# Kernel optimization log

Measured on AMD Instinct MI355X. Metric: run time of the kernel, lower is better.

The kernel has to match this reference:

```python
import jax, jax.numpy as jnp
import numpy as np


def _dwconv3(x, w, b):
    # Depthwise conv1d, kernel=3, 'same' padding, channels_first.
    # x: [B, Cs, L], w: [3, Cs], b: [Cs]
    xp = jnp.pad(x, ((0, 0), (0, 0), (1, 1)))
    return (w[0][:, None] * xp[:, :, :-2]
            + w[1][:, None] * xp[:, :, 1:-1]
            + w[2][:, None] * xp[:, :, 2:]
            + b[:, None])


def setup_inputs() -> dict:
    key = jax.random.key(0)
    ks = jax.random.split(key, 3)
    B, C, L, S = 32, 256, 4096, 8
    return {
        "inputs": jax.random.normal(ks[0], (B, C, L), jnp.float32),
        "conv_w": jax.random.normal(ks[1], (S, 3, C // S), jnp.float32) * 0.3,
        "conv_b": jnp.zeros((S, C // S), jnp.float32),
        "ln_gamma": jnp.ones((L,), jnp.float32),
        "ln_beta": jnp.zeros((L,), jnp.float32),
        "pw_w": jax.random.normal(ks[2], (C,), jnp.float32) * 0.3,
        "pw_b": jnp.zeros((C,), jnp.float32),
    }


def reference(inputs, conv_w, conv_b, ln_gamma, ln_beta, pw_w, pw_b):
    S = conv_w.shape[0]
    xs = jnp.split(inputs, S, axis=1)  # each [B, C/S, L]
    # sequential recurrence: y_i = dwconv_i(x_i + y_{i-1})
    y = _dwconv3(xs[0], conv_w[0], conv_b[0])
    ys = [y]
    for i in range(1, S):
        y = _dwconv3(xs[i] + y, conv_w[i], conv_b[i])
        ys.append(y)
    y = jnp.concatenate(ys, axis=1)  # [B, C, L]
    # keras LayerNormalization(axis=-1): normalize over time axis L
    mean = jnp.mean(y, axis=-1, keepdims=True)
    var = jnp.var(y, axis=-1, keepdims=True)
    y = (y - mean) * jax.lax.rsqrt(var + 1e-6) * ln_gamma + ln_beta
    # depthwise k=1 conv (per-channel scale + bias) then exact gelu
    y = jax.nn.gelu(y * pw_w[None, :, None] + pw_b[None, :, None], approximate=False)
    return inputs + y
```

## Files before the change

### kernel.cpp

```cpp
#include <hip/hip_runtime.h>
#include <math.h>

#define BB   32
#define CC   256
#define LL   4096
#define SS   8
#define CS   32
#define NT   512
#define NW   (NT / 64)
#define F4_ROW (LL / 4)
#define F4_THR (F4_ROW / NT)

__device__ __forceinline__ float gelu_exact(float x) {
    return 0.5f * x * (1.0f + erff(x * 0.70710678118654752440f));
}

__global__ __launch_bounds__(NT, 8)
void hdconv_encoder_kernel(const float* __restrict__ inp,
                           const float* __restrict__ conv_w,
                           const float* __restrict__ conv_b,
                           const float* __restrict__ ln_g,
                           const float* __restrict__ ln_b,
                           const float* __restrict__ pw_w,
                           const float* __restrict__ pw_b,
                           float* __restrict__ out) {
    __shared__ float4 S4[F4_ROW];
    __shared__ float  red[2 * NW];

    const int t    = threadIdx.x;
    const int blk  = blockIdx.x;
    const int b    = blk >> 5;
    const int c    = blk & 31;
    const int lane = t & 63;
    const int wave = t >> 6;

    float y[4 * F4_THR];
#pragma unroll
    for (int j = 0; j < 4 * F4_THR; ++j) y[j] = 0.0f;

    const float4* gp = (const float4*)ln_g;
    const float4* ep = (const float4*)ln_b;

    for (int i = 0; i < SS; ++i) {
        const int ch = i * CS + c;
        const float4* xrow = (const float4*)(inp + ((size_t)(b * CC + ch)) * LL);
        float4*       orow = (float4*)(out + ((size_t)(b * CC + ch)) * LL);

        float4 x4[F4_THR];
#pragma unroll
        for (int k = 0; k < F4_THR; ++k) x4[k] = xrow[t + NT * k];
        float4 g4[F4_THR], e4[F4_THR];
#pragma unroll
        for (int k = 0; k < F4_THR; ++k) {
            g4[k] = gp[t + NT * k];
            e4[k] = ep[t + NT * k];
        }
#pragma unroll
        for (int k = 0; k < F4_THR; ++k) {
            float4 s;
            s.x = x4[k].x + y[4 * k + 0];
            s.y = x4[k].y + y[4 * k + 1];
            s.z = x4[k].z + y[4 * k + 2];
            s.w = x4[k].w + y[4 * k + 3];
            S4[t + NT * k] = s;
        }
        __syncthreads();

        const float w0 = conv_w[i * 96 + 0 * CS + c];
        const float w1 = conv_w[i * 96 + 1 * CS + c];
        const float w2 = conv_w[i * 96 + 2 * CS + c];
        const float bb = conv_b[i * CS + c];

        float lsum = 0.0f, lsq = 0.0f;
#pragma unroll
        for (int k = 0; k < F4_THR; ++k) {
            const int f = t + NT * k;
            const float4 cc = S4[f];
            const float4 fm = S4[(f > 0) ? (f - 1) : 0];
            const float4 fp = S4[(f < F4_ROW - 1) ? (f + 1) : (F4_ROW - 1)];
            const float sm1 = (f > 0)          ? fm.w : 0.0f;
            const float sp4 = (f < F4_ROW - 1) ? fp.x : 0.0f;
            float y0 = fmaf(w0, sm1,  fmaf(w1, cc.x, fmaf(w2, cc.y, bb)));
            float y1 = fmaf(w0, cc.x, fmaf(w1, cc.y, fmaf(w2, cc.z, bb)));
            float y2 = fmaf(w0, cc.y, fmaf(w1, cc.z, fmaf(w2, cc.w, bb)));
            float y3 = fmaf(w0, cc.z, fmaf(w1, cc.w, fmaf(w2, sp4, bb)));
            y[4 * k + 0] = y0; y[4 * k + 1] = y1;
            y[4 * k + 2] = y2; y[4 * k + 3] = y3;
            lsum += (y0 + y1) + (y2 + y3);
            lsq  += fmaf(y0, y0, fmaf(y1, y1, fmaf(y2, y2, y3 * y3)));
        }

#pragma unroll
        for (int off = 32; off > 0; off >>= 1) {
            lsum += __shfl_down(lsum, off, 64);
            lsq  += __shfl_down(lsq,  off, 64);
        }
        if (lane == 0) { red[wave * 2] = lsum; red[wave * 2 + 1] = lsq; }
        __syncthreads();

        float sum = 0.0f, sq = 0.0f;
#pragma unroll
        for (int w = 0; w < NW; ++w) {
            sum += red[2 * w];
            sq  += red[2 * w + 1];
        }
        const float mean = sum * (1.0f / LL);
        const float var  = sq * (1.0f / LL) - mean * mean;
        const float inv  = rsqrtf(var + 1e-6f);

        const float pw = pw_w[ch];
        const float pb = pw_b[ch];
#pragma unroll
        for (int k = 0; k < F4_THR; ++k) {
            float4 o;
            float n;
            n   = fmaf((y[4 * k + 0] - mean) * inv, g4[k].x, e4[k].x);
            o.x = x4[k].x + gelu_exact(fmaf(n, pw, pb));
            n   = fmaf((y[4 * k + 1] - mean) * inv, g4[k].y, e4[k].y);
            o.y = x4[k].y + gelu_exact(fmaf(n, pw, pb));
            n   = fmaf((y[4 * k + 2] - mean) * inv, g4[k].z, e4[k].z);
            o.z = x4[k].z + gelu_exact(fmaf(n, pw, pb));
            n   = fmaf((y[4 * k + 3] - mean) * inv, g4[k].w, e4[k].w);
            o.w = x4[k].w + gelu_exact(fmaf(n, pw, pb));
            orow[t + NT * k] = o;
        }
    }
}

extern "C" void kernel_launch(void* const* d_in, const int* in_sizes, int n_in,
                              void* d_out, int out_size, void* d_ws, size_t ws_size,
                              hipStream_t stream) {
    const float* inp    = (const float*)d_in[0];
    const float* conv_w = (const float*)d_in[1];
    const float* conv_b = (const float*)d_in[2];
    const float* ln_g   = (const float*)d_in[3];
    const float* ln_b   = (const float*)d_in[4];
    const float* pw_w   = (const float*)d_in[5];
    const float* pw_b   = (const float*)d_in[6];
    float* out = (float*)d_out;

    dim3 grid(BB * CS);
    dim3 block(NT);
    hdconv_encoder_kernel<<<grid, block, 0, stream>>>(
        inp, conv_w, conv_b, ln_g, ln_b, pw_w, pw_b, out);
}
```

Before: 257.8 us.

## Halve block size, prefetch next split's input, use shuffles for conv halos

Halves the block to 256 threads so each thread holds 16 elements. The input row for the next split is prefetched into registers while the current split is processed, so the load overlaps the stencil, LayerNorm and GELU work. The full-row LDS staging of the convolution input is dropped: neighbor values now come from wave shuffles, with a small LDS seam array for wave boundaries, and barriers are replaced by a custom waitcnt-plus-barrier. The cost is higher register pressure, which may lower occupancy, and fewer threads per block.

```diff
diff --git a/kernel.cpp b/kernel.cpp
--- a/kernel.cpp
+++ b/kernel.cpp
@@ -6,16 +6,21 @@
 #define LL   4096
 #define SS   8
 #define CS   32
-#define NT   512
+#define NT   256
 #define NW   (NT / 64)
 #define F4_ROW (LL / 4)
 #define F4_THR (F4_ROW / NT)
+#define NSEG  (NW * F4_THR)
 
 __device__ __forceinline__ float gelu_exact(float x) {
     return 0.5f * x * (1.0f + erff(x * 0.70710678118654752440f));
 }
 
-__global__ __launch_bounds__(NT, 8)
+__device__ __forceinline__ void bar_lds() {
+    asm volatile("s_waitcnt lgkmcnt(0)\n\ts_barrier" ::: "memory");
+}
+
+__global__ __launch_bounds__(NT, 4)
 void hdconv_encoder_kernel(const float* __restrict__ inp,
                            const float* __restrict__ conv_w,
                            const float* __restrict__ conv_b,
@@ -24,8 +29,9 @@
                            const float* __restrict__ pw_w,
                            const float* __restrict__ pw_b,
                            float* __restrict__ out) {
-    __shared__ float4 S4[F4_ROW];
-    __shared__ float  red[2 * NW];
+    __shared__ float seamW[NSEG + 1];
+    __shared__ float seamX[NSEG + 1];
+    __shared__ float red[2 * NW];
 
     const int t    = threadIdx.x;
     const int blk  = blockIdx.x;
@@ -34,37 +40,57 @@
     const int lane = t & 63;
     const int wave = t >> 6;
 
-    float y[4 * F4_THR];
+    if (t == 0) { seamW[0] = 0.0f; seamX[NSEG] = 0.0f; }
+
+    float y[16];
 #pragma unroll
-    for (int j = 0; j < 4 * F4_THR; ++j) y[j] = 0.0f;
+    for (int j = 0; j < 16; ++j) y[j] = 0.0f;
 
-    const float4* gp = (const float4*)ln_g;
-    const float4* ep = (const float4*)ln_b;
-
-    for (int i = 0; i < SS; ++i) {
-        const int ch = i * CS + c;
-        const float4* xrow = (const float4*)(inp + ((size_t)(b * CC + ch)) * LL);
-        float4*       orow = (float4*)(out + ((size_t)(b * CC + ch)) * LL);
-
-        float4 x4[F4_THR];
-#pragma unroll
-        for (int k = 0; k < F4_THR; ++k) x4[k] = xrow[t + NT * k];
-        float4 g4[F4_THR], e4[F4_THR];
+    float4 g4[F4_THR], e4[F4_THR];
+    {
+        const float4* gp = (const float4*)ln_g;
+        const float4* ep = (const float4*)ln_b;
 #pragma unroll
         for (int k = 0; k < F4_THR; ++k) {
             g4[k] = gp[t + NT * k];
             e4[k] = ep[t + NT * k];
         }
+    }
+
+    float4 xc[F4_THR];
+    {
+        const float4* xrow = (const float4*)(inp + ((size_t)(b * CC + c)) * LL);
+#pragma unroll
+        for (int k = 0; k < F4_THR; ++k) xc[k] = xrow[t + NT * k];
+    }
+
+    for (int i = 0; i < SS; ++i) {
+        const int ch = i * CS + c;
+        float4* orow = (float4*)(out + ((size_t)(b * CC + ch)) * LL);
+
+        const int inext = (i < SS - 1) ? (i + 1) : i;
+        const float4* xnrow = (const float4*)(inp + ((size_t)(b * CC + inext * CS + c)) * LL);
+        float4 xn[F4_THR];
+#pragma unroll
+        for (int k = 0; k < F4_THR; ++k) xn[k] = xnrow[t + NT * k];
+
+        float4 s4[F4_THR];
 #pragma unroll
         for (int k = 0; k < F4_THR; ++k) {
-            float4 s;
-            s.x = x4[k].x + y[4 * k + 0];
-            s.y = x4[k].y + y[4 * k + 1];
-            s.z = x4[k].z + y[4 * k + 2];
-            s.w = x4[k].w + y[4 * k + 3];
-            S4[t + NT * k] = s;
+            s4[k].x = xc[k].x + y[4 * k + 0];
+            s4[k].y = xc[k].y + y[4 * k + 1];
+            s4[k].z = xc[k].z + y[4 * k + 2];
+            s4[k].w = xc[k].w + y[4 * k + 3];
         }
-        __syncthreads();
+        if (lane == 63) {
+#pragma unroll
+            for (int k = 0; k < F4_THR; ++k) seamW[1 + (k * NW + wave)] = s4[k].w;
+        }
+        if (lane == 0) {
+#pragma unroll
+            for (int k = 0; k < F4_THR; ++k) seamX[k * NW + wave] = s4[k].x;
+        }
+        bar_lds();
 
         const float w0 = conv_w[i * 96 + 0 * CS + c];
         const float w1 = conv_w[i * 96 + 1 * CS + c];
@@ -74,12 +100,12 @@
         float lsum = 0.0f, lsq = 0.0f;
 #pragma unroll
         for (int k = 0; k < F4_THR; ++k) {
-            const int f = t + NT * k;
-            const float4 cc = S4[f];
-            const float4 fm = S4[(f > 0) ? (f - 1) : 0];
-            const float4 fp = S4[(f < F4_ROW - 1) ? (f + 1) : (F4_ROW - 1)];
-            const float sm1 = (f > 0)          ? fm.w : 0.0f;
-            const float sp4 = (f < F4_ROW - 1) ? fp.x : 0.0f;
+            const int j = k * NW + wave;
+            float sm1 = __shfl_up(s4[k].w, 1);
+            float sp4 = __shfl_down(s4[k].x, 1);
+            if (lane == 0)  sm1 = seamW[j];
+            if (lane == 63) sp4 = seamX[j + 1];
+            const float4 cc = s4[k];
             float y0 = fmaf(w0, sm1,  fmaf(w1, cc.x, fmaf(w2, cc.y, bb)));
             float y1 = fmaf(w0, cc.x, fmaf(w1, cc.y, fmaf(w2, cc.z, bb)));
             float y2 = fmaf(w0, cc.y, fmaf(w1, cc.z, fmaf(w2, cc.w, bb)));
@@ -96,7 +122,7 @@
             lsq  += __shfl_down(lsq,  off, 64);
         }
         if (lane == 0) { red[wave * 2] = lsum; red[wave * 2 + 1] = lsq; }
-        __syncthreads();
+        bar_lds();
 
         float sum = 0.0f, sq = 0.0f;
 #pragma unroll
@@ -115,15 +141,18 @@
             float4 o;
             float n;
             n   = fmaf((y[4 * k + 0] - mean) * inv, g4[k].x, e4[k].x);
-            o.x = x4[k].x + gelu_exact(fmaf(n, pw, pb));
+            o.x = xc[k].x + gelu_exact(fmaf(n, pw, pb));
             n   = fmaf((y[4 * k + 1] - mean) * inv, g4[k].y, e4[k].y);
-            o.y = x4[k].y + gelu_exact(fmaf(n, pw, pb));
+            o.y = xc[k].y + gelu_exact(fmaf(n, pw, pb));
             n   = fmaf((y[4 * k + 2] - mean) * inv, g4[k].z, e4[k].z);
-            o.z = x4[k].z + gelu_exact(fmaf(n, pw, pb));
+            o.z = xc[k].z + gelu_exact(fmaf(n, pw, pb));
             n   = fmaf((y[4 * k + 3] - mean) * inv, g4[k].w, e4[k].w);
-            o.w = x4[k].w + gelu_exact(fmaf(n, pw, pb));
+            o.w = xc[k].w + gelu_exact(fmaf(n, pw, pb));
             orow[t + NT * k] = o;
         }
+
+#pragma unroll
+        for (int k = 0; k < F4_THR; ++k) xc[k] = xn[k];
     }
 }
 
```

Result: slower. 284.8 us (+10.5%).

## Split into halo-tiled stats and apply kernels for far more parallelism

Applied to the files above, without the earlier changes.

The single kernel ran one block per (batch, channel) chain over the full length, with block-wide syncs at every group step. It is replaced by two kernels that tile the length into 480-element cores with 16-element halos, one wave per tile. Each wave recomputes the 8-step conv recurrence in registers, using wave shuffles for neighbour values. The first kernel accumulates per-channel sum and sum-of-squares with atomics into a zeroed workspace, and the second recomputes the conv and applies layernorm, GELU and the residual. This trades a second read of the input, the redundant halo work and the atomics for much higher occupancy and no block-level synchronisation.

```diff
diff --git a/kernel.cpp b/kernel.cpp
--- a/kernel.cpp
+++ b/kernel.cpp
@@ -1,129 +1,190 @@
 #include <hip/hip_runtime.h>
 #include <math.h>
 
-#define BB   32
-#define CC   256
-#define LL   4096
-#define SS   8
-#define CS   32
-#define NT   512
-#define NW   (NT / 64)
-#define F4_ROW (LL / 4)
-#define F4_THR (F4_ROW / NT)
+#define BBATCH 32
+#define NCH    256
+#define LLEN   4096
+#define NGRP   8
+#define CSZ    32
+#define CORE   480
+#define HALO   16
+#define NTILE  9
+#define NCHAIN (BBATCH * CSZ)
+#define NWAVE  (NCHAIN * NTILE)
+#define NBLK   (NWAVE / 4)
 
 __device__ __forceinline__ float gelu_exact(float x) {
     return 0.5f * x * (1.0f + erff(x * 0.70710678118654752440f));
 }
 
-__global__ __launch_bounds__(NT, 8)
-void hdconv_encoder_kernel(const float* __restrict__ inp,
-                           const float* __restrict__ conv_w,
-                           const float* __restrict__ conv_b,
-                           const float* __restrict__ ln_g,
-                           const float* __restrict__ ln_b,
-                           const float* __restrict__ pw_w,
-                           const float* __restrict__ pw_b,
-                           float* __restrict__ out) {
-    __shared__ float4 S4[F4_ROW];
-    __shared__ float  red[2 * NW];
-
-    const int t    = threadIdx.x;
-    const int blk  = blockIdx.x;
-    const int b    = blk >> 5;
-    const int c    = blk & 31;
-    const int lane = t & 63;
-    const int wave = t >> 6;
-
-    float y[4 * F4_THR];
-#pragma unroll
-    for (int j = 0; j < 4 * F4_THR; ++j) y[j] = 0.0f;
-
-    const float4* gp = (const float4*)ln_g;
-    const float4* ep = (const float4*)ln_b;
-
-    for (int i = 0; i < SS; ++i) {
-        const int ch = i * CS + c;
-        const float4* xrow = (const float4*)(inp + ((size_t)(b * CC + ch)) * LL);
-        float4*       orow = (float4*)(out + ((size_t)(b * CC + ch)) * LL);
-
-        float4 x4[F4_THR];
-#pragma unroll
-        for (int k = 0; k < F4_THR; ++k) x4[k] = xrow[t + NT * k];
-        float4 g4[F4_THR], e4[F4_THR];
-#pragma unroll
-        for (int k = 0; k < F4_THR; ++k) {
-            g4[k] = gp[t + NT * k];
-            e4[k] = ep[t + NT * k];
-        }
-#pragma unroll
-        for (int k = 0; k < F4_THR; ++k) {
-            float4 s;
-            s.x = x4[k].x + y[4 * k + 0];
-            s.y = x4[k].y + y[4 * k + 1];
-            s.z = x4[k].z + y[4 * k + 2];
-            s.w = x4[k].w + y[4 * k + 3];
-            S4[t + NT * k] = s;
-        }
-        __syncthreads();
-
-        const float w0 = conv_w[i * 96 + 0 * CS + c];
-        const float w1 = conv_w[i * 96 + 1 * CS + c];
-        const float w2 = conv_w[i * 96 + 2 * CS + c];
-        const float bb = conv_b[i * CS + c];
-
-        float lsum = 0.0f, lsq = 0.0f;
-#pragma unroll
-        for (int k = 0; k < F4_THR; ++k) {
-            const int f = t + NT * k;
-            const float4 cc = S4[f];
-            const float4 fm = S4[(f > 0) ? (f - 1) : 0];
-            const float4 fp = S4[(f < F4_ROW - 1) ? (f + 1) : (F4_ROW - 1)];
-            const float sm1 = (f > 0)          ? fm.w : 0.0f;
-            const float sp4 = (f < F4_ROW - 1) ? fp.x : 0.0f;
-            float y0 = fmaf(w0, sm1,  fmaf(w1, cc.x, fmaf(w2, cc.y, bb)));
-            float y1 = fmaf(w0, cc.x, fmaf(w1, cc.y, fmaf(w2, cc.z, bb)));
-            float y2 = fmaf(w0, cc.y, fmaf(w1, cc.z, fmaf(w2, cc.w, bb)));
-            float y3 = fmaf(w0, cc.z, fmaf(w1, cc.w, fmaf(w2, sp4, bb)));
-            y[4 * k + 0] = y0; y[4 * k + 1] = y1;
-            y[4 * k + 2] = y2; y[4 * k + 3] = y3;
-            lsum += (y0 + y1) + (y2 + y3);
-            lsq  += fmaf(y0, y0, fmaf(y1, y1, fmaf(y2, y2, y3 * y3)));
-        }
-
-#pragma unroll
-        for (int off = 32; off > 0; off >>= 1) {
-            lsum += __shfl_down(lsum, off, 64);
-            lsq  += __shfl_down(lsq,  off, 64);
-        }
-        if (lane == 0) { red[wave * 2] = lsum; red[wave * 2 + 1] = lsq; }
-        __syncthreads();
-
-        float sum = 0.0f, sq = 0.0f;
-#pragma unroll
-        for (int w = 0; w < NW; ++w) {
-            sum += red[2 * w];
-            sq  += red[2 * w + 1];
-        }
-        const float mean = sum * (1.0f / LL);
-        const float var  = sq * (1.0f / LL) - mean * mean;
+struct TileGeom {
+    int b, c, t, l;
+    int p0, q0;
+    bool force0;
+    bool coreval;
+};
+
+__device__ __forceinline__ TileGeom tile_geom(int blockId, int tid) {
+    TileGeom g;
+    g.l = tid & 63;
+    int wid = blockId * 4 + (tid >> 6);
+    g.t = wid % NTILE;
+    int chain = wid / NTILE;
+    g.c = chain & 31;
+    g.b = chain >> 5;
+    g.p0 = g.t * CORE - HALO + 8 * g.l;
+    int q = g.p0 < 0 ? 0 : g.p0;
+    g.q0 = q > LLEN - 8 ? LLEN - 8 : q;
+    g.force0 = (g.p0 < 0) || (g.p0 >= LLEN);
+    const int coreLo = g.t * CORE;
+    const int coreHi = (coreLo + CORE > LLEN) ? LLEN : (coreLo + CORE);
+    g.coreval = (g.p0 >= coreLo) && (g.p0 < coreHi);
+    return g;
+}
+
+__device__ __forceinline__ void conv_step(const float* x, const float* yp, float* y,
+                                          bool force0, float w0, float w1, float w2,
+                                          float bc) {
+    float s[8];
+#pragma unroll
+    for (int j = 0; j < 8; ++j) s[j] = force0 ? 0.0f : (x[j] + yp[j]);
+    const float sL = __shfl_up(s[7], 1, 64);
+    const float sR = __shfl_down(s[0], 1, 64);
+    y[0] = fmaf(w0, sL,   fmaf(w1, s[0], fmaf(w2, s[1], bc)));
+#pragma unroll
+    for (int j = 1; j < 7; ++j)
+        y[j] = fmaf(w0, s[j - 1], fmaf(w1, s[j], fmaf(w2, s[j + 1], bc)));
+    y[7] = fmaf(w0, s[6], fmaf(w1, s[7], fmaf(w2, sR, bc)));
+}
+
+__global__ __launch_bounds__(256, 6)
+void k1_stats(const float* __restrict__ inp,
+              const float* __restrict__ conv_w,
+              const float* __restrict__ conv_b,
+              float* __restrict__ stats) {
+    const TileGeom g = tile_geom(blockIdx.x, threadIdx.x);
+
+    float yp[8], y[8], x[8], aS[8], aQ[8];
+#pragma unroll
+    for (int j = 0; j < 8; ++j) yp[j] = 0.0f;
+
+    const float4* rp0 = (const float4*)(inp + ((size_t)((g.b << 8) + g.c)) * LLEN) + (g.q0 >> 2);
+    float4 xA = rp0[0], xB = rp0[1];
+
+#pragma unroll
+    for (int i = 0; i < NGRP; ++i) {
+        float4 nA, nB;
+        if (i < NGRP - 1) {
+            const float4* np = (const float4*)(inp + ((size_t)((g.b << 8) + (i + 1) * CSZ + g.c)) * LLEN) + (g.q0 >> 2);
+            nA = np[0]; nB = np[1];
+        }
+        x[0] = xA.x; x[1] = xA.y; x[2] = xA.z; x[3] = xA.w;
+        x[4] = xB.x; x[5] = xB.y; x[6] = xB.z; x[7] = xB.w;
+
+        const float w0 = conv_w[i * 96 + g.c];
+        const float w1 = conv_w[i * 96 + 32 + g.c];
+        const float w2 = conv_w[i * 96 + 64 + g.c];
+        const float bc = conv_b[i * 32 + g.c];
+        conv_step(x, yp, y, g.force0, w0, w1, w2, bc);
+
+        float s1 = 0.0f, s2 = 0.0f;
+#pragma unroll
+        for (int j = 0; j < 8; ++j) { s1 += y[j]; s2 = fmaf(y[j], y[j], s2); }
+        aS[i] = s1; aQ[i] = s2;
+#pragma unroll
+        for (int j = 0; j < 8; ++j) yp[j] = y[j];
+        if (i < NGRP - 1) { xA = nA; xB = nB; }
+    }
+
+    if (!g.coreval) {
+#pragma unroll
+        for (int i = 0; i < 8; ++i) { aS[i] = 0.0f; aQ[i] = 0.0f; }
+    }
+#pragma unroll
+    for (int m = 1; m < 64; m <<= 1) {
+#pragma unroll
+        for (int i = 0; i < 8; ++i) {
+            aS[i] += __shfl_xor(aS[i], m, 64);
+            aQ[i] += __shfl_xor(aQ[i], m, 64);
+        }
+    }
+    if (g.l == 0) {
+#pragma unroll
+        for (int i = 0; i < 8; ++i) {
+            const int idx = (g.b << 8) + (i << 5) + g.c;
+            atomicAdd(&stats[2 * idx],     aS[i]);
+            atomicAdd(&stats[2 * idx + 1], aQ[i]);
+        }
+    }
+}
+
+__global__ __launch_bounds__(256, 4)
+void k2_apply(const float* __restrict__ inp,
+              const float* __restrict__ conv_w,
+              const float* __restrict__ conv_b,
+              const float* __restrict__ ln_g,
+              const float* __restrict__ ln_b,
+              const float* __restrict__ pw_w,
+              const float* __restrict__ pw_b,
+              const float* __restrict__ stats,
+              float* __restrict__ out) {
+    const TileGeom g = tile_geom(blockIdx.x, threadIdx.x);
+
+    const float4* gp = (const float4*)ln_g + (g.q0 >> 2);
+    const float4* ep = (const float4*)ln_b + (g.q0 >> 2);
+    const float4 gA = gp[0], gB = gp[1];
+    const float4 eA = ep[0], eB = ep[1];
+    float gam[8] = {gA.x, gA.y, gA.z, gA.w, gB.x, gB.y, gB.z, gB.w};
+    float bet[8] = {eA.x, eA.y, eA.z, eA.w, eB.x, eB.y, eB.z, eB.w};
+
+    float yp[8], y[8], x[8];
+#pragma unroll
+    for (int j = 0; j < 8; ++j) yp[j] = 0.0f;
+
+    const float4* rp0 = (const float4*)(inp + ((size_t)((g.b << 8) + g.c)) * LLEN) + (g.q0 >> 2);
+    float4 xA = rp0[0], xB = rp0[1];
+
+#pragma unroll
+    for (int i = 0; i < NGRP; ++i) {
+        float4 nA, nB;
+        if (i < NGRP - 1) {
+            const float4* np = (const float4*)(inp + ((size_t)((g.b << 8) + (i + 1) * CSZ + g.c)) * LLEN) + (g.q0 >> 2);
+            nA = np[0]; nB = np[1];
+        }
+        x[0] = xA.x; x[1] = xA.y; x[2] = xA.z; x[3] = xA.w;
+        x[4] = xB.x; x[5] = xB.y; x[6] = xB.z; x[7] = xB.w;
+
+        const int ch = (i << 5) + g.c;
+        const float w0 = conv_w[i * 96 + g.c];
+        const float w1 = conv_w[i * 96 + 32 + g.c];
+        const float w2 = conv_w[i * 96 + 64 + g.c];
+        const float bc = conv_b[i * 32 + g.c];
+        conv_step(x, yp, y, g.force0, w0, w1, w2, bc);
+
+        const int idx = (g.b << 8) + ch;
+        const float S = stats[2 * idx];
+        const float Q = stats[2 * idx + 1];
+        const float mean = S * (1.0f / LLEN);
+        const float var  = fmaf(-mean, mean, Q * (1.0f / LLEN));
         const float inv  = rsqrtf(var + 1e-6f);
-
-        const float pw = pw_w[ch];
-        const float pb = pw_b[ch];
-#pragma unroll
-        for (int k = 0; k < F4_THR; ++k) {
-            float4 o;
-            float n;
-            n   = fmaf((y[4 * k + 0] - mean) * inv, g4[k].x, e4[k].x);
-            o.x = x4[k].x + gelu_exact(fmaf(n, pw, pb));
-            n   = fmaf((y[4 * k + 1] - mean) * inv, g4[k].y, e4[k].y);
-            o.y = x4[k].y + gelu_exact(fmaf(n, pw, pb));
-            n   = fmaf((y[4 * k + 2] - mean) * inv, g4[k].z, e4[k].z);
-            o.z = x4[k].z + gelu_exact(fmaf(n, pw, pb));
-            n   = fmaf((y[4 * k + 3] - mean) * inv, g4[k].w, e4[k].w);
-            o.w = x4[k].w + gelu_exact(fmaf(n, pw, pb));
-            orow[t + NT * k] = o;
-        }
+        const float pwv  = pw_w[ch];
+        const float pbv  = pw_b[ch];
+
+        if (g.coreval) {
+            float o[8];
+#pragma unroll
+            for (int j = 0; j < 8; ++j) {
+                const float n = fmaf((y[j] - mean) * inv, gam[j], bet[j]);
+                o[j] = x[j] + gelu_exact(fmaf(n, pwv, pbv));
+            }
+            float4* op = (float4*)(out + ((size_t)((g.b << 8) + ch)) * LLEN) + (g.q0 >> 2);
+            op[0] = make_float4(o[0], o[1], o[2], o[3]);
+            op[1] = make_float4(o[4], o[5], o[6], o[7]);
+        }
+
+#pragma unroll
+        for (int j = 0; j < 8; ++j) yp[j] = y[j];
+        if (i < NGRP - 1) { xA = nA; xB = nB; }
     }
 }
 
@@ -137,10 +198,11 @@
     const float* ln_b   = (const float*)d_in[4];
     const float* pw_w   = (const float*)d_in[5];
     const float* pw_b   = (const float*)d_in[6];
-    float* out = (float*)d_out;
-
-    dim3 grid(BB * CS);
-    dim3 block(NT);
-    hdconv_encoder_kernel<<<grid, block, 0, stream>>>(
-        inp, conv_w, conv_b, ln_g, ln_b, pw_w, pw_b, out);
-}
+    float* out   = (float*)d_out;
+    float* stats = (float*)d_ws;
+
+    hipMemsetAsync(d_ws, 0, BBATCH * NCH * 2 * sizeof(float), stream);
+    k1_stats<<<NBLK, 256, 0, stream>>>(inp, conv_w, conv_b, stats);
+    k2_apply<<<NBLK, 256, 0, stream>>>(inp, conv_w, conv_b, ln_g, ln_b,
+                                       pw_w, pw_b, stats, out);
+}
```

New measurement: 266.8 us. 3.5% more time.
